# Kernel tuning notes

Hardware: AMD Instinct MI355X
Metric: run time of the kernel (lower is better)

Reference implementation:

```python
import jax, jax.numpy as jnp
import numpy as np

B, H, S, D = 2, 16, 2048, 128
TEMPERATURE = 11.313708498984761  # sqrt(128)


def setup_inputs() -> dict:
    key = jax.random.key(0)
    kq, kk, kv = jax.random.split(key, 3)
    q = jax.random.normal(kq, (B, H, S, D), dtype=jnp.float32)
    k = jax.random.normal(kk, (B, H, S, D), dtype=jnp.float32)
    v = jax.random.normal(kv, (B, H, S, D), dtype=jnp.float32)
    # causal (lower-triangular) mask; 0 == masked, matching mask.eq(0) semantics
    mask = jnp.broadcast_to(
        jnp.tril(jnp.ones((S, S), dtype=jnp.int32))[None, None], (B, 1, S, S)
    )
    return {"q": q, "k": k, "v": v, "mask": mask}


def reference(q, k, v, mask):
    # attn = q @ k^T / temperature   -> [B,H,S,S]
    attn = jnp.einsum("bhqd,bhkd->bhqk", q, k) / TEMPERATURE
    masked = mask == 0  # True where masked out
    attn = jnp.where(masked, -jnp.inf, attn)
    attn = jax.nn.softmax(attn, axis=-1)
    attn = jnp.where(masked, 0.0, attn)
    # output = attn @ v -> [B,H,S,D]
    return jnp.einsum("bhqk,bhkd->bhqd", attn, v)
```

## Files before the change

### kernel.cpp

```cpp
#include <hip/hip_runtime.h>
#include <hip/hip_bf16.h>

#define NB   2
#define NH   16
#define NBH  (NB*NH)
#define SEQ  2048
#define DH   128

#define KBLK 64
#define QB   64
#define QW   16
#define KS   136
#define VS   72
#define PS   72

typedef short  short8    __attribute__((ext_vector_type(8)));
typedef unsigned short ushort8_t __attribute__((ext_vector_type(8)));
typedef float  f32x4     __attribute__((ext_vector_type(4)));
typedef int    int4v     __attribute__((ext_vector_type(4)));

constexpr float INV_T = 0.08838834764831845f;
constexpr float LOG2E = 1.4426950408889634f;
constexpr float QSCL  = INV_T * LOG2E;
constexpr float NEG   = -1e30f;
constexpr float DEFER = 8.0f;

__device__ __forceinline__ unsigned short f2b(float x) {
    union { float f; unsigned u; } c; c.f = x;
    unsigned r = c.u + 0x7FFFu + ((c.u >> 16) & 1u);
    return (unsigned short)(r >> 16);
}

__device__ __forceinline__ unsigned pack2(float lo, float hi) {
    return (unsigned)f2b(lo) | ((unsigned)f2b(hi) << 16);
}

__device__ __forceinline__ void gload_lds16(const void* g, void* l) {
    __builtin_amdgcn_global_load_lds(
        (const __attribute__((address_space(1))) unsigned int*)g,
        (__attribute__((address_space(3))) unsigned int*)l, 16, 0, 0);
}

__global__ __launch_bounds__(256)
void prep_k(const float* __restrict__ K, unsigned short* __restrict__ Kb) {
    size_t i = ((size_t)blockIdx.x * 256 + threadIdx.x) * 8;
    float4 a = *(const float4*)(K + i);
    float4 b = *(const float4*)(K + i + 4);
    ushort8_t o;
    o[0]=f2b(a.x); o[1]=f2b(a.y); o[2]=f2b(a.z); o[3]=f2b(a.w);
    o[4]=f2b(b.x); o[5]=f2b(b.y); o[6]=f2b(b.z); o[7]=f2b(b.w);
    *(ushort8_t*)(Kb + i) = o;
}

__global__ __launch_bounds__(256)
void prep_v(const float* __restrict__ V, unsigned short* __restrict__ Vt) {
    __shared__ unsigned short T[64][72];
    const int bid = blockIdx.x;
    const int dt = bid & 1, st = (bid >> 1) & 31, bh = bid >> 6;
    const int s0 = st * 64, d0 = dt * 64;
    const float* vb = V + (size_t)bh * SEQ * DH;
    const int tid = threadIdx.x;
    #pragma unroll
    for (int u = 0; u < 4; ++u) {
        int f = tid + 256 * u;
        int sl = f >> 4, c4 = f & 15;
        float4 x = *(const float4*)(vb + (size_t)(s0 + sl) * DH + d0 + c4 * 4);
        T[c4*4+0][sl] = f2b(x.x); T[c4*4+1][sl] = f2b(x.y);
        T[c4*4+2][sl] = f2b(x.z); T[c4*4+3][sl] = f2b(x.w);
    }
    __syncthreads();
    unsigned short* vo = Vt + (size_t)bh * DH * SEQ;
    const int dr = tid >> 2, ch = tid & 3;
    ushort8_t w0 = *(const ushort8_t*)&T[dr][ch*16];
    ushort8_t w1 = *(const ushort8_t*)&T[dr][ch*16 + 8];
    *(ushort8_t*)(vo + (size_t)(d0+dr)*SEQ + s0 + ch*16)     = w0;
    *(ushort8_t*)(vo + (size_t)(d0+dr)*SEQ + s0 + ch*16 + 8) = w1;
}

__global__ __launch_bounds__(256, 2)
void attn_fwd2(const float* __restrict__ Q,
               const unsigned short* __restrict__ Kb,
               const unsigned short* __restrict__ Vt,
               float* __restrict__ O)
{
    __shared__ __align__(16) unsigned short Ksh[2][64 * 128];
    __shared__ __align__(16) unsigned short Vsh[2][128 * 64];

    const int bid  = blockIdx.x;
    const int pair = bid & 15;
    const int bh   = bid >> 4;
    const int tid  = threadIdx.x;
    const int wid  = tid >> 6;
    const int lane = tid & 63;
    const int l15  = lane & 15;
    const int l4   = lane >> 4;
    const int rx   = l15 & 7;
    const int hi   = l4 >> 1;
    const int srcA = l15 + 16 * ((2 * l4) & 3);
    const int srcB = l15 + 16 * ((2 * l4 + 1) & 3);

    const size_t base = (size_t)bh * SEQ * DH;
    const unsigned short* Kbh = Kb + base;
    const unsigned short* Vth = Vt + base;

    auto stage = [&](int bufi, int tt) {
        const int kv0 = tt * KBLK;
        {
            const int sl = lane & 15, rr = lane >> 4;
            #pragma unroll
            for (int i = 0; i < 4; ++i) {
                int row = wid * 16 + i * 4 + rr;
                int ss  = sl ^ (row & 7);
                gload_lds16(Kbh + (size_t)(kv0 + row) * DH + ss * 8,
                            &Ksh[bufi][(wid * 16 + i * 4) * 128]);
            }
        }
        {
            const int sl = lane & 7, rr = lane >> 3;
            #pragma unroll
            for (int i = 0; i < 4; ++i) {
                int row = wid * 32 + i * 8 + rr;
                int ss  = sl ^ (row & 7);
                gload_lds16(Vth + (size_t)row * SEQ + kv0 + ss * 8,
                            &Vsh[bufi][(wid * 32 + i * 8) * 64]);
            }
        }
    };

    for (int ph = 0; ph < 2; ++ph) {
        const int qblk  = ph ? (31 - pair) : pair;
        const int qbase = qblk * 64 + wid * QW;
        const int nt    = qblk + 1;
        const int qrow  = qbase + l15;

        short8 aq[4];
        {
            const float* qp = Q + base + (size_t)qrow * DH + 8 * l4;
            #pragma unroll
            for (int kb = 0; kb < 4; ++kb) {
                float4 x0 = *(const float4*)(qp + 32 * kb);
                float4 x1 = *(const float4*)(qp + 32 * kb + 4);
                short8 a;
                a[0] = (short)f2b(x0.x * QSCL); a[1] = (short)f2b(x0.y * QSCL);
                a[2] = (short)f2b(x0.z * QSCL); a[3] = (short)f2b(x0.w * QSCL);
                a[4] = (short)f2b(x1.x * QSCL); a[5] = (short)f2b(x1.y * QSCL);
                a[6] = (short)f2b(x1.z * QSCL); a[7] = (short)f2b(x1.w * QSCL);
                aq[kb] = a;
            }
        }

        f32x4 acc[8];
        #pragma unroll
        for (int i = 0; i < 8; ++i) acc[i] = (f32x4){0.f, 0.f, 0.f, 0.f};
        float mrun = NEG, lrun = 0.f;

        __syncthreads();
        stage(0, 0);

        for (int t = 0; t < nt; ++t) {
            const int cur = t & 1;
            const int kvb = t * KBLK;
            asm volatile("s_waitcnt vmcnt(0)" ::: "memory");
            __syncthreads();
            if (t + 1 < nt) stage(cur ^ 1, t + 1);

            const unsigned short* Kc = Ksh[cur];
            const unsigned short* Vc = Vsh[cur];

            f32x4 sf[4];
            __builtin_amdgcn_s_setprio(1);
            #pragma unroll
            for (int f = 0; f < 4; ++f) {
                f32x4 c = (f32x4){0.f, 0.f, 0.f, 0.f};
                const int row = 16 * f + l15;
                #pragma unroll
                for (int kb = 0; kb < 4; ++kb) {
                    short8 bk = *(const short8*)&Kc[row * 128 + ((4 * kb + l4) ^ rx) * 8];
                    c = __builtin_amdgcn_mfma_f32_16x16x32_bf16(bk, aq[kb], c, 0, 0, 0);
                }
                sf[f] = c;
            }
            __builtin_amdgcn_s_setprio(0);

            if (kvb + KBLK - 1 > qbase) {
                #pragma unroll
                for (int f = 0; f < 4; ++f) {
                    #pragma unroll
                    for (int j = 0; j < 4; ++j) {
                        const int kv = kvb + 16 * f + 4 * l4 + j;
                        if (kv > qrow) sf[f][j] = NEG;
                    }
                }
            }

            float pmax;
            {
                float m0 = fmaxf(fmaxf(sf[0][0], sf[0][1]), fmaxf(sf[0][2], sf[0][3]));
                float m1 = fmaxf(fmaxf(sf[1][0], sf[1][1]), fmaxf(sf[1][2], sf[1][3]));
                float m2 = fmaxf(fmaxf(sf[2][0], sf[2][1]), fmaxf(sf[2][2], sf[2][3]));
                float m3 = fmaxf(fmaxf(sf[3][0], sf[3][1]), fmaxf(sf[3][2], sf[3][3]));
                pmax = fmaxf(fmaxf(m0, m1), fmaxf(m2, m3));
            }
            pmax = fmaxf(pmax, __shfl_xor(pmax, 16));
            pmax = fmaxf(pmax, __shfl_xor(pmax, 32));

            if (__any(pmax > mrun + DEFER)) {
                float mn  = fmaxf(mrun, pmax);
                float scl = exp2f(mrun - mn);
                mrun = mn;
                lrun *= scl;
                #pragma unroll
                for (int i = 0; i < 8; ++i)
                    #pragma unroll
                    for (int j = 0; j < 4; ++j)
                        acc[i][j] *= scl;
            }

            float rs = 0.f;
            #pragma unroll
            for (int f = 0; f < 4; ++f)
                #pragma unroll
                for (int j = 0; j < 4; ++j) {
                    float p = exp2f(sf[f][j] - mrun);
                    sf[f][j] = p;
                    rs += p;
                }
            rs += __shfl_xor(rs, 16);
            rs += __shfl_xor(rs, 32);
            lrun += rs;

            unsigned pd0[4], pd1[4];
            #pragma unroll
            for (int f = 0; f < 4; ++f) {
                pd0[f] = pack2(sf[f][0], sf[f][1]);
                pd1[f] = pack2(sf[f][2], sf[f][3]);
            }

            #pragma unroll
            for (int kb = 0; kb < 2; ++kb) {
                unsigned sA0 = __shfl(pd0[2*kb],     srcA);
                unsigned sA1 = __shfl(pd1[2*kb],     srcA);
                unsigned tA0 = __shfl(pd0[2*kb + 1], srcA);
                unsigned tA1 = __shfl(pd1[2*kb + 1], srcA);
                unsigned sB0 = __shfl(pd0[2*kb],     srcB);
                unsigned sB1 = __shfl(pd1[2*kb],     srcB);
                unsigned tB0 = __shfl(pd0[2*kb + 1], srcB);
                unsigned tB1 = __shfl(pd1[2*kb + 1], srcB);
                int4v w;
                w[0] = (int)(hi ? tA0 : sA0);
                w[1] = (int)(hi ? tA1 : sA1);
                w[2] = (int)(hi ? tB0 : sB0);
                w[3] = (int)(hi ? tB1 : sB1);
                short8 pb;
                __builtin_memcpy(&pb, &w, 16);

                __builtin_amdgcn_s_setprio(1);
                #pragma unroll
                for (int db = 0; db < 8; ++db) {
                    const int row = 16 * db + l15;
                    short8 bv = *(const short8*)&Vc[row * 64 + ((4 * kb + l4) ^ rx) * 8];
                    acc[db] = __builtin_amdgcn_mfma_f32_16x16x32_bf16(bv, pb, acc[db], 0, 0, 0);
                }
                __builtin_amdgcn_s_setprio(0);
            }
        }

        const float inv = 1.f / lrun;
        float* op = O + base + (size_t)qrow * DH + 4 * l4;
        #pragma unroll
        for (int db = 0; db < 8; ++db) {
            float4 v;
            v.x = acc[db][0] * inv; v.y = acc[db][1] * inv;
            v.z = acc[db][2] * inv; v.w = acc[db][3] * inv;
            *(float4*)(op + 16 * db) = v;
        }
    }
}

__global__ __launch_bounds__(256)
void attn_fwd(const float* __restrict__ Q, const float* __restrict__ K,
              const float* __restrict__ V, float* __restrict__ O)
{
    __shared__ __align__(16) unsigned short KshL[KBLK * KS];
    __shared__ __align__(16) unsigned short VshL[DH * VS];
    __shared__ __align__(16) unsigned short PshL[4][QW * PS];

    const int bid  = blockIdx.x;
    const int qblk = bid & 31;
    const int bh   = bid >> 5;
    const int tid  = threadIdx.x;
    const int wid  = tid >> 6;
    const int lane = tid & 63;
    const int l15  = lane & 15;
    const int l4   = lane >> 4;

    const size_t base  = (size_t)bh * SEQ * DH;
    const int    qbase = qblk * QB + wid * QW;

    short8 aq[4];
    {
        const float* qp = Q + base + (size_t)(qbase + l15) * DH + 8 * l4;
        #pragma unroll
        for (int kb = 0; kb < 4; ++kb) {
            float4 x0 = *(const float4*)(qp + 32 * kb);
            float4 x1 = *(const float4*)(qp + 32 * kb + 4);
            short8 a;
            a[0] = (short)f2b(x0.x * INV_T); a[1] = (short)f2b(x0.y * INV_T);
            a[2] = (short)f2b(x0.z * INV_T); a[3] = (short)f2b(x0.w * INV_T);
            a[4] = (short)f2b(x1.x * INV_T); a[5] = (short)f2b(x1.y * INV_T);
            a[6] = (short)f2b(x1.z * INV_T); a[7] = (short)f2b(x1.w * INV_T);
            aq[kb] = a;
        }
    }
    f32x4 acc[8];
    #pragma unroll
    for (int i = 0; i < 8; ++i) acc[i] = (f32x4){0.f, 0.f, 0.f, 0.f};
    float mrun[4], lrun[4];
    #pragma unroll
    for (int j = 0; j < 4; ++j) { mrun[j] = NEG; lrun[j] = 0.f; }

    const int ntiles = qblk + 1;
    for (int t = 0; t < ntiles; ++t) {
        const int kvb = t * KBLK;
        #pragma unroll
        for (int i = 0; i < 8; ++i) {
            int f  = tid + 256 * i;
            int kv = f >> 5, c4 = f & 31;
            float4 x = *(const float4*)(K + base + (size_t)(kvb + kv) * DH + 4 * c4);
            ushort4 b4;
            b4.x = f2b(x.x); b4.y = f2b(x.y); b4.z = f2b(x.z); b4.w = f2b(x.w);
            *(ushort4*)&KshL[kv * KS + 4 * c4] = b4;
        }
        {
            const int dd  = tid & 127;
            const int kvg = (tid >> 7) * 8;
            #pragma unroll
            for (int p = 0; p < 4; ++p) {
                const int kvL = p * 16 + kvg;
                const float* vp = V + base + (size_t)(kvb + kvL) * DH + dd;
                float x[8];
                #pragma unroll
                for (int j = 0; j < 8; ++j) x[j] = vp[(size_t)j * DH];
                ushort4 lo, hi;
                lo.x = f2b(x[0]); lo.y = f2b(x[1]); lo.z = f2b(x[2]); lo.w = f2b(x[3]);
                hi.x = f2b(x[4]); hi.y = f2b(x[5]); hi.z = f2b(x[6]); hi.w = f2b(x[7]);
                *(ushort4*)&VshL[dd * VS + kvL]     = lo;
                *(ushort4*)&VshL[dd * VS + kvL + 4] = hi;
            }
        }
        __syncthreads();
        if (kvb <= qbase + QW - 1) {
            f32x4 sf[4];
            #pragma unroll
            for (int f = 0; f < 4; ++f) {
                f32x4 c = (f32x4){0.f, 0.f, 0.f, 0.f};
                #pragma unroll
                for (int kb = 0; kb < 4; ++kb) {
                    short8 bk = *(const short8*)&KshL[(16 * f + l15) * KS + 32 * kb + 8 * l4];
                    c = __builtin_amdgcn_mfma_f32_16x16x32_bf16(aq[kb], bk, c, 0, 0, 0);
                }
                sf[f] = c;
            }
            float pmax[4] = {NEG, NEG, NEG, NEG};
            #pragma unroll
            for (int f = 0; f < 4; ++f) {
                const int col = kvb + 16 * f + l15;
                #pragma unroll
                for (int j = 0; j < 4; ++j) {
                    const int row = qbase + 4 * l4 + j;
                    float val = (col <= row) ? sf[f][j] : NEG;
                    sf[f][j] = val;
                    pmax[j] = fmaxf(pmax[j], val);
                }
            }
            #pragma unroll
            for (int j = 0; j < 4; ++j) {
                #pragma unroll
                for (int off = 8; off > 0; off >>= 1)
                    pmax[j] = fmaxf(pmax[j], __shfl_xor(pmax[j], off));
            }
            float scl[4], rsum[4];
            #pragma unroll
            for (int j = 0; j < 4; ++j) {
                float mn = fmaxf(mrun[j], pmax[j]);
                scl[j]  = exp2f((mrun[j] - mn) * LOG2E);
                mrun[j] = mn;
                rsum[j] = 0.f;
            }
            #pragma unroll
            for (int f = 0; f < 4; ++f) {
                #pragma unroll
                for (int j = 0; j < 4; ++j) {
                    float pv = exp2f((sf[f][j] - mrun[j]) * LOG2E);
                    sf[f][j] = pv;
                    rsum[j] += pv;
                }
            }
            #pragma unroll
            for (int j = 0; j < 4; ++j) {
                #pragma unroll
                for (int off = 8; off > 0; off >>= 1)
                    rsum[j] += __shfl_xor(rsum[j], off);
                lrun[j] = lrun[j] * scl[j] + rsum[j];
            }
            #pragma unroll
            for (int i = 0; i < 8; ++i)
                #pragma unroll
                for (int j = 0; j < 4; ++j)
                    acc[i][j] *= scl[j];
            #pragma unroll
            for (int f = 0; f < 4; ++f)
                #pragma unroll
                for (int j = 0; j < 4; ++j)
                    PshL[wid][(4 * l4 + j) * PS + 16 * f + l15] = f2b(sf[f][j]);
            #pragma unroll
            for (int kb = 0; kb < 2; ++kb) {
                short8 pa = *(const short8*)&PshL[wid][l15 * PS + 32 * kb + 8 * l4];
                #pragma unroll
                for (int db = 0; db < 8; ++db) {
                    short8 bv = *(const short8*)&VshL[(16 * db + l15) * VS + 32 * kb + 8 * l4];
                    acc[db] = __builtin_amdgcn_mfma_f32_16x16x32_bf16(pa, bv, acc[db], 0, 0, 0);
                }
            }
        }
        __syncthreads();
    }
    float inv[4];
    #pragma unroll
    for (int j = 0; j < 4; ++j) inv[j] = 1.f / lrun[j];
    float* op = O + base + (size_t)qbase * DH;
    #pragma unroll
    for (int db = 0; db < 8; ++db)
        #pragma unroll
        for (int j = 0; j < 4; ++j)
            op[(size_t)(4 * l4 + j) * DH + 16 * db + l15] = acc[db][j] * inv[j];
}

extern "C" void kernel_launch(void* const* d_in, const int* in_sizes, int n_in,
                              void* d_out, int out_size, void* d_ws, size_t ws_size,
                              hipStream_t stream) {
    const float* q = (const float*)d_in[0];
    const float* k = (const float*)d_in[1];
    const float* v = (const float*)d_in[2];
    float* o = (float*)d_out;

    const size_t elems = (size_t)NBH * SEQ * DH;
    const size_t need  = elems * 2 * sizeof(unsigned short);
    if (ws_size >= need) {
        unsigned short* Kb = (unsigned short*)d_ws;
        unsigned short* Vt = Kb + elems;
        prep_k<<<dim3((unsigned)(elems / (256 * 8))), dim3(256), 0, stream>>>(k, Kb);
        prep_v<<<dim3(NBH * (SEQ / 64) * (DH / 64)), dim3(256), 0, stream>>>(v, Vt);
        attn_fwd2<<<dim3(NBH * 16), dim3(256), 0, stream>>>(q, Kb, Vt, o);
    } else {
        attn_fwd<<<dim3(NBH * 32), dim3(256), 0, stream>>>(q, k, v, o);
    }
}
```

Measured before the change: 240.2 us.

## Process 128-row Q tiles per block with two row groups per wave

The attention kernel now gives each block a single 128-row query tile, with each wave handling two 16-row groups instead of looping over a paired light/heavy 64-row tile. Each K/V tile staged into LDS is reused for twice as many query rows, roughly halving LDS reads per MFMA. The P·V product switches to 16x16x16 bf16 MFMAs so the softmax output feeds directly from registers without the cross-lane shuffle repacking. Blocks are ordered heaviest-first to balance causal work. In exchange, register pressure roughly doubles (two accumulator sets), and blocks are unbalanced without the pairing trick.

```diff
diff --git a/kernel.cpp b/kernel.cpp
--- a/kernel.cpp
+++ b/kernel.cpp
@@ -15,9 +15,9 @@
 #define PS   72
 
 typedef short  short8    __attribute__((ext_vector_type(8)));
+typedef short  short4v   __attribute__((ext_vector_type(4)));
 typedef unsigned short ushort8_t __attribute__((ext_vector_type(8)));
 typedef float  f32x4     __attribute__((ext_vector_type(4)));
-typedef int    int4v     __attribute__((ext_vector_type(4)));
 
 constexpr float INV_T = 0.08838834764831845f;
 constexpr float LOG2E = 1.4426950408889634f;
@@ -33,6 +33,21 @@
 
 __device__ __forceinline__ unsigned pack2(float lo, float hi) {
     return (unsigned)f2b(lo) | ((unsigned)f2b(hi) << 16);
+}
+
+__device__ __forceinline__ short4v mk4(unsigned lo, unsigned hi) {
+    union { unsigned u[2]; short4v s; } x; x.u[0] = lo; x.u[1] = hi; return x.s;
+}
+
+__device__ __forceinline__ f32x4 mfma16(short4v a, short4v b, f32x4 c) {
+#if __has_builtin(__builtin_amdgcn_mfma_f32_16x16x16bf16_1k)
+    return __builtin_amdgcn_mfma_f32_16x16x16bf16_1k(a, b, c, 0, 0, 0);
+#else
+    f32x4 d;
+    asm("v_mfma_f32_16x16x16_bf16 %0, %1, %2, %3"
+        : "=v"(d) : "v"(a), "v"(b), "0"(c));
+    return d;
+#endif
 }
 
 __device__ __forceinline__ void gload_lds16(const void* g, void* l) {
@@ -78,7 +93,7 @@
 }
 
 __global__ __launch_bounds__(256, 2)
-void attn_fwd2(const float* __restrict__ Q,
+void attn_fwd3(const float* __restrict__ Q,
                const unsigned short* __restrict__ Kb,
                const unsigned short* __restrict__ Vt,
                float* __restrict__ O)
@@ -87,21 +102,23 @@
     __shared__ __align__(16) unsigned short Vsh[2][128 * 64];
 
     const int bid  = blockIdx.x;
-    const int pair = bid & 15;
-    const int bh   = bid >> 4;
+    const int qblk = 15 - (bid >> 5);
+    const int bh   = bid & 31;
     const int tid  = threadIdx.x;
     const int wid  = tid >> 6;
     const int lane = tid & 63;
     const int l15  = lane & 15;
     const int l4   = lane >> 4;
     const int rx   = l15 & 7;
-    const int hi   = l4 >> 1;
-    const int srcA = l15 + 16 * ((2 * l4) & 3);
-    const int srcB = l15 + 16 * ((2 * l4 + 1) & 3);
 
     const size_t base = (size_t)bh * SEQ * DH;
     const unsigned short* Kbh = Kb + base;
     const unsigned short* Vth = Vt + base;
+
+    const int qbase = qblk * 128 + wid * 32;
+    const int nt    = 2 * qblk + 2;
+    const int qr0   = qbase + l15;
+    const int qr1   = qbase + 16 + l15;
 
     auto stage = [&](int bufi, int tt) {
         const int kv0 = tt * KBLK;
@@ -127,58 +144,65 @@
         }
     };
 
-    for (int ph = 0; ph < 2; ++ph) {
-        const int qblk  = ph ? (31 - pair) : pair;
-        const int qbase = qblk * 64 + wid * QW;
-        const int nt    = qblk + 1;
-        const int qrow  = qbase + l15;
-
-        short8 aq[4];
-        {
-            const float* qp = Q + base + (size_t)qrow * DH + 8 * l4;
-            #pragma unroll
-            for (int kb = 0; kb < 4; ++kb) {
-                float4 x0 = *(const float4*)(qp + 32 * kb);
-                float4 x1 = *(const float4*)(qp + 32 * kb + 4);
-                short8 a;
-                a[0] = (short)f2b(x0.x * QSCL); a[1] = (short)f2b(x0.y * QSCL);
-                a[2] = (short)f2b(x0.z * QSCL); a[3] = (short)f2b(x0.w * QSCL);
-                a[4] = (short)f2b(x1.x * QSCL); a[5] = (short)f2b(x1.y * QSCL);
-                a[6] = (short)f2b(x1.z * QSCL); a[7] = (short)f2b(x1.w * QSCL);
-                aq[kb] = a;
-            }
-        }
-
-        f32x4 acc[8];
+    short8 aq0[4], aq1[4];
+    {
+        const float* qp0 = Q + base + (size_t)qr0 * DH + 8 * l4;
+        const float* qp1 = Q + base + (size_t)qr1 * DH + 8 * l4;
         #pragma unroll
-        for (int i = 0; i < 8; ++i) acc[i] = (f32x4){0.f, 0.f, 0.f, 0.f};
-        float mrun = NEG, lrun = 0.f;
-
+        for (int kb = 0; kb < 4; ++kb) {
+            float4 x0 = *(const float4*)(qp0 + 32 * kb);
+            float4 x1 = *(const float4*)(qp0 + 32 * kb + 4);
+            float4 y0 = *(const float4*)(qp1 + 32 * kb);
+            float4 y1 = *(const float4*)(qp1 + 32 * kb + 4);
+            short8 a, b;
+            a[0] = (short)f2b(x0.x * QSCL); a[1] = (short)f2b(x0.y * QSCL);
+            a[2] = (short)f2b(x0.z * QSCL); a[3] = (short)f2b(x0.w * QSCL);
+            a[4] = (short)f2b(x1.x * QSCL); a[5] = (short)f2b(x1.y * QSCL);
+            a[6] = (short)f2b(x1.z * QSCL); a[7] = (short)f2b(x1.w * QSCL);
+            b[0] = (short)f2b(y0.x * QSCL); b[1] = (short)f2b(y0.y * QSCL);
+            b[2] = (short)f2b(y0.z * QSCL); b[3] = (short)f2b(y0.w * QSCL);
+            b[4] = (short)f2b(y1.x * QSCL); b[5] = (short)f2b(y1.y * QSCL);
+            b[6] = (short)f2b(y1.z * QSCL); b[7] = (short)f2b(y1.w * QSCL);
+            aq0[kb] = a; aq1[kb] = b;
+        }
+    }
+
+    f32x4 acc0[8], acc1[8];
+    #pragma unroll
+    for (int i = 0; i < 8; ++i) {
+        acc0[i] = (f32x4){0.f, 0.f, 0.f, 0.f};
+        acc1[i] = (f32x4){0.f, 0.f, 0.f, 0.f};
+    }
+    float mrun0 = NEG, lrun0 = 0.f;
+    float mrun1 = NEG, lrun1 = 0.f;
+
+    stage(0, 0);
+
+    for (int t = 0; t < nt; ++t) {
+        const int cur = t & 1;
+        const int kvb = t * KBLK;
+        asm volatile("s_waitcnt vmcnt(0)" ::: "memory");
         __syncthreads();
-        stage(0, 0);
-
-        for (int t = 0; t < nt; ++t) {
-            const int cur = t & 1;
-            const int kvb = t * KBLK;
-            asm volatile("s_waitcnt vmcnt(0)" ::: "memory");
-            __syncthreads();
-            if (t + 1 < nt) stage(cur ^ 1, t + 1);
-
+        if (t + 1 < nt) stage(cur ^ 1, t + 1);
+
+        if (kvb <= qbase + 31) {
             const unsigned short* Kc = Ksh[cur];
             const unsigned short* Vc = Vsh[cur];
 
-            f32x4 sf[4];
+            f32x4 sf0[4], sf1[4];
             __builtin_amdgcn_s_setprio(1);
             #pragma unroll
             for (int f = 0; f < 4; ++f) {
-                f32x4 c = (f32x4){0.f, 0.f, 0.f, 0.f};
+                f32x4 c0 = (f32x4){0.f, 0.f, 0.f, 0.f};
+                f32x4 c1 = (f32x4){0.f, 0.f, 0.f, 0.f};
                 const int row = 16 * f + l15;
                 #pragma unroll
                 for (int kb = 0; kb < 4; ++kb) {
                     short8 bk = *(const short8*)&Kc[row * 128 + ((4 * kb + l4) ^ rx) * 8];
-                    c = __builtin_amdgcn_mfma_f32_16x16x32_bf16(bk, aq[kb], c, 0, 0, 0);
-                }
-                sf[f] = c;
+                    c0 = __builtin_amdgcn_mfma_f32_16x16x32_bf16(bk, aq0[kb], c0, 0, 0, 0);
+                    c1 = __builtin_amdgcn_mfma_f32_16x16x32_bf16(bk, aq1[kb], c1, 0, 0, 0);
+                }
+                sf0[f] = c0; sf1[f] = c1;
             }
             __builtin_amdgcn_s_setprio(0);
 
@@ -188,92 +212,92 @@
                     #pragma unroll
                     for (int j = 0; j < 4; ++j) {
                         const int kv = kvb + 16 * f + 4 * l4 + j;
-                        if (kv > qrow) sf[f][j] = NEG;
+                        if (kv > qr0) sf0[f][j] = NEG;
+                        if (kv > qr1) sf1[f][j] = NEG;
                     }
                 }
             }
 
-            float pmax;
+            float pmax0, pmax1;
             {
-                float m0 = fmaxf(fmaxf(sf[0][0], sf[0][1]), fmaxf(sf[0][2], sf[0][3]));
-                float m1 = fmaxf(fmaxf(sf[1][0], sf[1][1]), fmaxf(sf[1][2], sf[1][3]));
-                float m2 = fmaxf(fmaxf(sf[2][0], sf[2][1]), fmaxf(sf[2][2], sf[2][3]));
-                float m3 = fmaxf(fmaxf(sf[3][0], sf[3][1]), fmaxf(sf[3][2], sf[3][3]));
-                pmax = fmaxf(fmaxf(m0, m1), fmaxf(m2, m3));
-            }
-            pmax = fmaxf(pmax, __shfl_xor(pmax, 16));
-            pmax = fmaxf(pmax, __shfl_xor(pmax, 32));
-
-            if (__any(pmax > mrun + DEFER)) {
-                float mn  = fmaxf(mrun, pmax);
-                float scl = exp2f(mrun - mn);
-                mrun = mn;
-                lrun *= scl;
+                float a0 = fmaxf(fmaxf(sf0[0][0], sf0[0][1]), fmaxf(sf0[0][2], sf0[0][3]));
+                float a1 = fmaxf(fmaxf(sf0[1][0], sf0[1][1]), fmaxf(sf0[1][2], sf0[1][3]));
+                float a2 = fmaxf(fmaxf(sf0[2][0], sf0[2][1]), fmaxf(sf0[2][2], sf0[2][3]));
+                float a3 = fmaxf(fmaxf(sf0[3][0], sf0[3][1]), fmaxf(sf0[3][2], sf0[3][3]));
+                pmax0 = fmaxf(fmaxf(a0, a1), fmaxf(a2, a3));
+                float b0 = fmaxf(fmaxf(sf1[0][0], sf1[0][1]), fmaxf(sf1[0][2], sf1[0][3]));
+                float b1 = fmaxf(fmaxf(sf1[1][0], sf1[1][1]), fmaxf(sf1[1][2], sf1[1][3]));
+                float b2 = fmaxf(fmaxf(sf1[2][0], sf1[2][1]), fmaxf(sf1[2][2], sf1[2][3]));
+                float b3 = fmaxf(fmaxf(sf1[3][0], sf1[3][1]), fmaxf(sf1[3][2], sf1[3][3]));
+                pmax1 = fmaxf(fmaxf(b0, b1), fmaxf(b2, b3));
+            }
+            pmax0 = fmaxf(pmax0, __shfl_xor(pmax0, 16));
+            pmax0 = fmaxf(pmax0, __shfl_xor(pmax0, 32));
+            pmax1 = fmaxf(pmax1, __shfl_xor(pmax1, 16));
+            pmax1 = fmaxf(pmax1, __shfl_xor(pmax1, 32));
+
+            if (__any((pmax0 > mrun0 + DEFER) || (pmax1 > mrun1 + DEFER))) {
+                float mn0 = fmaxf(mrun0, pmax0), mn1 = fmaxf(mrun1, pmax1);
+                float s0 = exp2f(mrun0 - mn0),   s1 = exp2f(mrun1 - mn1);
+                mrun0 = mn0; mrun1 = mn1;
+                lrun0 *= s0; lrun1 *= s1;
                 #pragma unroll
                 for (int i = 0; i < 8; ++i)
                     #pragma unroll
-                    for (int j = 0; j < 4; ++j)
-                        acc[i][j] *= scl;
-            }
-
-            float rs = 0.f;
-            #pragma unroll
-            for (int f = 0; f < 4; ++f)
-                #pragma unroll
-                for (int j = 0; j < 4; ++j) {
-                    float p = exp2f(sf[f][j] - mrun);
-                    sf[f][j] = p;
-                    rs += p;
-                }
-            rs += __shfl_xor(rs, 16);
-            rs += __shfl_xor(rs, 32);
-            lrun += rs;
-
-            unsigned pd0[4], pd1[4];
-            #pragma unroll
-            for (int f = 0; f < 4; ++f) {
-                pd0[f] = pack2(sf[f][0], sf[f][1]);
-                pd1[f] = pack2(sf[f][2], sf[f][3]);
-            }
-
-            #pragma unroll
-            for (int kb = 0; kb < 2; ++kb) {
-                unsigned sA0 = __shfl(pd0[2*kb],     srcA);
-                unsigned sA1 = __shfl(pd1[2*kb],     srcA);
-                unsigned tA0 = __shfl(pd0[2*kb + 1], srcA);
-                unsigned tA1 = __shfl(pd1[2*kb + 1], srcA);
-                unsigned sB0 = __shfl(pd0[2*kb],     srcB);
-                unsigned sB1 = __shfl(pd1[2*kb],     srcB);
-                unsigned tB0 = __shfl(pd0[2*kb + 1], srcB);
-                unsigned tB1 = __shfl(pd1[2*kb + 1], srcB);
-                int4v w;
-                w[0] = (int)(hi ? tA0 : sA0);
-                w[1] = (int)(hi ? tA1 : sA1);
-                w[2] = (int)(hi ? tB0 : sB0);
-                w[3] = (int)(hi ? tB1 : sB1);
-                short8 pb;
-                __builtin_memcpy(&pb, &w, 16);
-
+                    for (int j = 0; j < 4; ++j) {
+                        acc0[i][j] *= s0;
+                        acc1[i][j] *= s1;
+                    }
+            }
+
+            unsigned pa0[4], pb0_[4], pa1[4], pb1_[4];
+            float rs0 = 0.f, rs1 = 0.f;
+            #pragma unroll
+            for (int f = 0; f < 4; ++f) {
+                float p00 = exp2f(sf0[f][0] - mrun0), p01 = exp2f(sf0[f][1] - mrun0);
+                float p02 = exp2f(sf0[f][2] - mrun0), p03 = exp2f(sf0[f][3] - mrun0);
+                float p10 = exp2f(sf1[f][0] - mrun1), p11 = exp2f(sf1[f][1] - mrun1);
+                float p12 = exp2f(sf1[f][2] - mrun1), p13 = exp2f(sf1[f][3] - mrun1);
+                rs0 += (p00 + p01) + (p02 + p03);
+                rs1 += (p10 + p11) + (p12 + p13);
+                pa0[f]  = pack2(p00, p01); pb0_[f] = pack2(p02, p03);
+                pa1[f]  = pack2(p10, p11); pb1_[f] = pack2(p12, p13);
+            }
+            rs0 += __shfl_xor(rs0, 16); rs0 += __shfl_xor(rs0, 32);
+            rs1 += __shfl_xor(rs1, 16); rs1 += __shfl_xor(rs1, 32);
+            lrun0 += rs0; lrun1 += rs1;
+
+            #pragma unroll
+            for (int f = 0; f < 4; ++f) {
+                short4v pf0 = mk4(pa0[f], pb0_[f]);
+                short4v pf1 = mk4(pa1[f], pb1_[f]);
                 __builtin_amdgcn_s_setprio(1);
                 #pragma unroll
                 for (int db = 0; db < 8; ++db) {
                     const int row = 16 * db + l15;
-                    short8 bv = *(const short8*)&Vc[row * 64 + ((4 * kb + l4) ^ rx) * 8];
-                    acc[db] = __builtin_amdgcn_mfma_f32_16x16x32_bf16(bv, pb, acc[db], 0, 0, 0);
+                    short4v va = *(const short4v*)
+                        &Vc[row * 64 + ((2 * f + (l4 >> 1)) ^ rx) * 8 + (l4 & 1) * 4];
+                    acc0[db] = mfma16(va, pf0, acc0[db]);
+                    acc1[db] = mfma16(va, pf1, acc1[db]);
                 }
                 __builtin_amdgcn_s_setprio(0);
             }
         }
-
-        const float inv = 1.f / lrun;
-        float* op = O + base + (size_t)qrow * DH + 4 * l4;
-        #pragma unroll
-        for (int db = 0; db < 8; ++db) {
-            float4 v;
-            v.x = acc[db][0] * inv; v.y = acc[db][1] * inv;
-            v.z = acc[db][2] * inv; v.w = acc[db][3] * inv;
-            *(float4*)(op + 16 * db) = v;
-        }
+    }
+
+    const float inv0 = 1.f / lrun0;
+    const float inv1 = 1.f / lrun1;
+    float* op0 = O + base + (size_t)qr0 * DH + 4 * l4;
+    float* op1 = O + base + (size_t)qr1 * DH + 4 * l4;
+    #pragma unroll
+    for (int db = 0; db < 8; ++db) {
+        float4 v0, v1;
+        v0.x = acc0[db][0] * inv0; v0.y = acc0[db][1] * inv0;
+        v0.z = acc0[db][2] * inv0; v0.w = acc0[db][3] * inv0;
+        v1.x = acc1[db][0] * inv1; v1.y = acc1[db][1] * inv1;
+        v1.z = acc1[db][2] * inv1; v1.w = acc1[db][3] * inv1;
+        *(float4*)(op0 + 16 * db) = v0;
+        *(float4*)(op1 + 16 * db) = v1;
     }
 }
 
@@ -451,7 +475,7 @@
         unsigned short* Vt = Kb + elems;
         prep_k<<<dim3((unsigned)(elems / (256 * 8))), dim3(256), 0, stream>>>(k, Kb);
         prep_v<<<dim3(NBH * (SEQ / 64) * (DH / 64)), dim3(256), 0, stream>>>(v, Vt);
-        attn_fwd2<<<dim3(NBH * 16), dim3(256), 0, stream>>>(q, Kb, Vt, o);
+        attn_fwd3<<<dim3(NBH * 16), dim3(256), 0, stream>>>(q, Kb, Vt, o);
     } else {
         attn_fwd<<<dim3(NBH * 32), dim3(256), 0, stream>>>(q, k, v, o);
     }
```

New measurement: 245.7 us. 2.3% more time.
